# Kernel optimization log

Measured on AMD Instinct MI355X. Metric: run time of the kernel, lower is better.

The kernel has to match this reference:

```python
import jax, jax.numpy as jnp
import numpy as np

B, N, E, D = 4, 4096, 4096, 128
NEG_SLOPE = 0.01
BN_EPS = 1e-5


def setup_inputs() -> dict:
    key = jax.random.key(0)
    ks = jax.random.split(key, 8)
    return {
        "incident_mat": (jax.random.uniform(ks[0], (B, N, E)) < 0.01).astype(jnp.float32),
        "degree_v": jax.random.normal(ks[1], (B, N, N), jnp.float32) * 0.01,
        "degree_e": jax.random.normal(ks[2], (B, E, E), jnp.float32) * 0.01,
        "x": jax.random.normal(ks[3], (B, N, D), jnp.float32),
        "e_masks": jax.random.randint(ks[4], (B, E), 0, 2, jnp.int32),
        "mlp_W": jax.random.normal(ks[5], (D, D), jnp.float32) / np.sqrt(D),
        "mlp_b": jnp.zeros((D,), jnp.float32),
        "theta_att": jax.random.normal(ks[6], (D, 1), jnp.float32) / np.sqrt(D),
        "eps": jax.random.uniform(ks[7], (1,), jnp.float32),
        "bn_gamma": jnp.ones((D,), jnp.float32),
        "bn_beta": jnp.zeros((D,), jnp.float32),
        "bn_mean": jnp.zeros((D,), jnp.float32),
        "bn_var": jnp.ones((D,), jnp.float32),
    }


def reference(incident_mat, degree_v, degree_e, x, e_masks, mlp_W, mlp_b,
              theta_att, eps, bn_gamma, bn_beta, bn_mean, bn_var):
    # MLP (num_mlp_layers=1 -> single Linear)
    x_w = x @ mlp_W + mlp_b                      # [B,N,D]
    Ht = jnp.swapaxes(incident_mat, 1, 2)        # [B,E,N]
    ht_x_w = Ht @ x_w                            # [B,E,D]
    # attention logits per hyperedge
    ht_x_theta = (Ht @ (x @ theta_att))[..., 0]  # [B,E]
    scores = jnp.where(e_masks == 0, -jnp.inf, ht_x_theta)
    attn = jax.nn.softmax(scores, axis=1)        # [B,E]
    # diag_embed + bmm == elementwise row scaling
    h1 = attn[..., None] * ht_x_w                # [B,E,D]
    h1 = incident_mat @ h1                       # [B,N,D]
    h1 = degree_v @ h1                           # [B,N,D]
    h1 = Ht @ h1                                 # [B,E,D]
    h1 = degree_e @ h1                           # [B,E,D]
    h = h1 + eps * ht_x_w                        # [B,E,D]
    h = incident_mat @ h                         # [B,N,D]
    h = jnp.where(h >= 0, h, NEG_SLOPE * h)      # leaky_relu; dropout=identity (eval)
    # BatchNorm1d over channels (inference mode)
    h = (h - bn_mean) / jnp.sqrt(bn_var + BN_EPS) * bn_gamma + bn_beta
    return h
```

## Files before the change

### kernel.cpp

```cpp
#include <hip/hip_runtime.h>


typedef __bf16 bf16;
typedef bf16 bf16x8 __attribute__((ext_vector_type(8)));
typedef float f32x4 __attribute__((ext_vector_type(4)));
typedef unsigned long long u64;
typedef unsigned short u16;
typedef u16 u16x8 __attribute__((ext_vector_type(8)));

#define LDK 72
#define SWZ(r, c) ((c) ^ ((((r) >> 3) & 7) << 3))
#define CAP 192

union BPack { bf16 h[2]; unsigned int u; };
static __device__ __forceinline__ bf16 tob(float f) { return (bf16)f; }

__global__ __launch_bounds__(256) void mlp_k(const float* __restrict__ x,
                                             const float* __restrict__ W,
                                             const float* __restrict__ bias,
                                             const float* __restrict__ theta,
                                             float* __restrict__ xw,
                                             float* __restrict__ xt) {
    __shared__ float Ws[32][128];
    __shared__ float xs[32][128];
    const int t = threadIdx.x;
    const long r0 = (long)blockIdx.x * 32;

    for (int i = t * 4; i < 4096; i += 1024)
        *(float4*)&xs[i >> 7][i & 127] = *(const float4*)&x[r0 * 128 + i];

    const int d = t & 127;
    const int rg = (t >> 7) * 16;
    float acc[16];
#pragma unroll
    for (int r = 0; r < 16; ++r) acc[r] = 0.f;

    for (int kk = 0; kk < 128; kk += 32) {
        __syncthreads();
        for (int i = t * 4; i < 4096; i += 1024)
            *(float4*)&Ws[i >> 7][i & 127] =
                *(const float4*)&W[(kk + (i >> 7)) * 128 + (i & 127)];
        __syncthreads();
        for (int k = 0; k < 32; ++k) {
            float w = Ws[k][d];
#pragma unroll
            for (int r = 0; r < 16; ++r) acc[r] += xs[rg + r][kk + k] * w;
        }
    }
    const float bd = bias[d];
#pragma unroll
    for (int r = 0; r < 16; ++r)
        xw[(r0 + rg + r) * 128 + d] = acc[r] + bd;

    if (t < 32) {
        float s = 0.f;
        for (int k = 0; k < 128; ++k) s += xs[t][k] * theta[k];
        xt[r0 + t] = s;
    }
}

__global__ __launch_bounds__(256) void bmask_lists_k(const float* __restrict__ inc,
                                                     u64* __restrict__ rowmask,
                                                     u16* __restrict__ idx,
                                                     int* __restrict__ cnts) {
    const int b = blockIdx.y;
    const int n = blockIdx.x * 4 + (threadIdx.x >> 6);
    const int l = threadIdx.x & 63;
    const float* p = inc + ((long)b << 24) + (long)n * 4096 + l * 64;
    u64 w = 0;
#pragma unroll
    for (int j = 0; j < 16; ++j) {
        const float4 v = *(const float4*)(p + j * 4);
        w |= (u64)(v.x != 0.f ? 1u : 0u) << (4 * j);
        w |= (u64)(v.y != 0.f ? 1u : 0u) << (4 * j + 1);
        w |= (u64)(v.z != 0.f ? 1u : 0u) << (4 * j + 2);
        w |= (u64)(v.w != 0.f ? 1u : 0u) << (4 * j + 3);
    }
    const long rowid = (long)b * 4096 + n;
    rowmask[rowid * 64 + l] = w;

    const int pc = __popcll(w);
    int pre = pc;
#pragma unroll
    for (int o = 1; o < 64; o <<= 1) {
        int t = __shfl_up(pre, o);
        if (l >= o) pre += t;
    }
    if (l == 63) cnts[rowid] = pre;
    u16* op = idx + rowid * CAP;
    int k = pre - pc;
    u64 m = w;
    while (m) {
        const int bit = __builtin_ctzll(m);
        m &= m - 1;
        if (k < CAP) op[k] = (u16)(l * 64 + bit);
        ++k;
    }
}

__global__ void btrans_k(const u64* __restrict__ rowmask, u64* __restrict__ colmask) {
    const int tn = blockIdx.x, te = blockIdx.y, b = blockIdx.z;
    const int l = threadIdx.x;
    __shared__ u64 w[64];
    w[l] = rowmask[((long)b * 4096 + tn * 64 + l) * 64 + te];
    __syncthreads();
    u64 o = 0;
#pragma unroll 8
    for (int j = 0; j < 64; ++j) o |= ((w[j] >> l) & 1ull) << j;
    colmask[((long)b * 4096 + te * 64 + l) * 64 + tn] = o;
}

__global__ __launch_bounds__(256) void lists_k(const u64* __restrict__ mask,
                                               u16* __restrict__ idx,
                                               int* __restrict__ cnts) {
    const int b = blockIdx.y;
    const int r = blockIdx.x * 4 + (threadIdx.x >> 6);
    const int l = threadIdx.x & 63;
    u64 m = mask[((long)b * 4096 + r) * 64 + l];
    const int pc = __popcll(m);
    int pre = pc;
#pragma unroll
    for (int o = 1; o < 64; o <<= 1) {
        int t = __shfl_up(pre, o);
        if (l >= o) pre += t;
    }
    if (l == 63) cnts[b * 4096 + r] = pre;
    u16* op = idx + ((long)b * 4096 + r) * CAP;
    int k = pre - pc;
    while (m) {
        const int bit = __builtin_ctzll(m);
        m &= m - 1;
        if (k < CAP) op[k] = (u16)(l * 64 + bit);
        ++k;
    }
}

__global__ void softmax_k(const float* __restrict__ sc, const int* __restrict__ mask,
                          float* __restrict__ attn) {
    const int b = blockIdx.x, t = threadIdx.x;
    __shared__ float red[1024];
    const float* sb = sc + b * 4096;
    const int* mb = mask + b * 4096;

    float mx = -1e30f;
    for (int e = t; e < 4096; e += 1024)
        if (mb[e] != 0) mx = fmaxf(mx, sb[e]);
    red[t] = mx;
    __syncthreads();
    for (int st = 512; st > 0; st >>= 1) {
        if (t < st) red[t] = fmaxf(red[t], red[t + st]);
        __syncthreads();
    }
    mx = red[0];
    __syncthreads();

    float sum = 0.f;
    for (int e = t; e < 4096; e += 1024)
        if (mb[e] != 0) sum += expf(sb[e] - mx);
    red[t] = sum;
    __syncthreads();
    for (int st = 512; st > 0; st >>= 1) {
        if (t < st) red[t] += red[t + st];
        __syncthreads();
    }
    const float inv = 1.f / red[0];
    for (int e = t; e < 4096; e += 1024)
        attn[b * 4096 + e] = (mb[e] != 0) ? expf(sb[e] - mx) * inv : 0.f;
}

__global__ __launch_bounds__(256) void scale_k(const float* __restrict__ hxw,
                                               const float* __restrict__ att,
                                               float* __restrict__ outp) {
    const long i4 = (long)blockIdx.x * 256 + threadIdx.x;
    float4 v = ((const float4*)hxw)[i4];
    const float s = att[i4 >> 5];
    v.x *= s; v.y *= s; v.z *= s; v.w *= s;
    ((float4*)outp)[i4] = v;
}

template <int KSP, bool EPS>
__global__ __launch_bounds__(256) void pairsum_k(const float* __restrict__ P,
                                                 const float* __restrict__ H,
                                                 const float* __restrict__ epsp,
                                                 float* __restrict__ O) {
    const long i4 = (long)blockIdx.x * 256 + threadIdx.x;
    float4 a = ((const float4*)P)[i4];
#pragma unroll
    for (int s = 1; s < KSP; ++s) {
        float4 c = ((const float4*)P)[i4 + (long)s * 524288];
        a.x += c.x; a.y += c.y; a.z += c.z; a.w += c.w;
    }
    if (EPS) {
        const float e = epsp[0];
        float4 h = ((const float4*)H)[i4];
        a.x += e * h.x; a.y += e * h.y; a.z += e * h.z; a.w += e * h.w;
    }
    ((float4*)O)[i4] = a;
}

template <bool HXT, bool EPI>
__global__ __launch_bounds__(256) void gatherE_k(
    const u16* __restrict__ idx, const int* __restrict__ cnts,
    const u64* __restrict__ mask, const float* __restrict__ src,
    const float* __restrict__ xt,
    const float* __restrict__ bng, const float* __restrict__ bnb,
    const float* __restrict__ bnm, const float* __restrict__ bnv,
    float* __restrict__ out, float* __restrict__ hxt) {
    const int bid = blockIdx.x;
    const int slot = bid & 7;
    const int b = slot >> 1;
    const int chunk = (bid >> 3) * 2 + (slot & 1);
    const int r = chunk * 4 + (threadIdx.x >> 6);
    const int l = threadIdx.x & 63;
    const long rowid = (long)b * 4096 + r;
    const int cnt = cnts[rowid];
    const u16* ip = idx + rowid * CAP;
    const float* S = src + (long)b * 524288;
    const float* xb = xt + (long)b * 4096;
    const int c0 = 2 * l;

    float ax0 = 0.f, ax1 = 0.f, ax2 = 0.f, ax3 = 0.f;
    float ax4 = 0.f, ax5 = 0.f, ax6 = 0.f, ax7 = 0.f;
    float ay0 = 0.f, ay1 = 0.f, ay2 = 0.f, ay3 = 0.f;
    float ay4 = 0.f, ay5 = 0.f, ay6 = 0.f, ay7 = 0.f;
    float hacc = 0.f;

    const int n = cnt < CAP ? cnt : CAP;
    int i = 0;
    if (n >= 8) {
        u16x8 ia = *(const u16x8*)ip;
        for (; i + 8 <= n; i += 8) {
            const int e0 = ia[0], e1 = ia[1], e2 = ia[2], e3 = ia[3];
            const int e4 = ia[4], e5 = ia[5], e6 = ia[6], e7 = ia[7];
            const float2 v0 = *(const float2*)(S + (long)e0 * 128 + c0);
            const float2 v1 = *(const float2*)(S + (long)e1 * 128 + c0);
            const float2 v2 = *(const float2*)(S + (long)e2 * 128 + c0);
            const float2 v3 = *(const float2*)(S + (long)e3 * 128 + c0);
            const float2 v4 = *(const float2*)(S + (long)e4 * 128 + c0);
            const float2 v5 = *(const float2*)(S + (long)e5 * 128 + c0);
            const float2 v6 = *(const float2*)(S + (long)e6 * 128 + c0);
            const float2 v7 = *(const float2*)(S + (long)e7 * 128 + c0);
            const bool more = (i + 16 <= n);
            u16x8 ib;
            if (more) ib = *(const u16x8*)(ip + i + 8);
            if (HXT)
                hacc += ((xb[e0] + xb[e1]) + (xb[e2] + xb[e3])) +
                        ((xb[e4] + xb[e5]) + (xb[e6] + xb[e7]));
            ax0 += v0.x; ay0 += v0.y; ax1 += v1.x; ay1 += v1.y;
            ax2 += v2.x; ay2 += v2.y; ax3 += v3.x; ay3 += v3.y;
            ax4 += v4.x; ay4 += v4.y; ax5 += v5.x; ay5 += v5.y;
            ax6 += v6.x; ay6 += v6.y; ax7 += v7.x; ay7 += v7.y;
            if (more) ia = ib;
        }
    }
    for (; i < n; ++i) {
        const int e = ip[i];
        const float2 v = *(const float2*)(S + (long)e * 128 + c0);
        if (HXT) hacc += xb[e];
        ax0 += v.x; ay0 += v.y;
    }

    if (cnt > CAP) {
        const u64 wrd = mask[rowid * 64 + l];
        int seen = 0;
        for (int wi = 0; wi < 64; ++wi) {
            u64 m = __shfl(wrd, wi);
            const int pc = __popcll(m);
            if (seen + pc > CAP) {
                int tk = CAP - seen;
                if (tk < 0) tk = 0;
                for (int t = 0; t < tk; ++t) m &= m - 1;
                while (m) {
                    const int bit = __builtin_ctzll(m);
                    m &= m - 1;
                    const int e = (wi << 6) + bit;
                    const float2 v = *(const float2*)(S + (long)e * 128 + c0);
                    if (HXT) hacc += xb[e];
                    ax0 += v.x; ay0 += v.y;
                }
            }
            seen += pc;
        }
    }

    float ax = ((ax0 + ax1) + (ax2 + ax3)) + ((ax4 + ax5) + (ax6 + ax7));
    float ay = ((ay0 + ay1) + (ay2 + ay3)) + ((ay4 + ay5) + (ay6 + ay7));
    if (EPI) {
        float t0 = (ax >= 0.f) ? ax : 0.01f * ax;
        float t1 = (ay >= 0.f) ? ay : 0.01f * ay;
        ax = (t0 - bnm[c0]) * rsqrtf(bnv[c0] + 1e-5f) * bng[c0] + bnb[c0];
        ay = (t1 - bnm[c0 + 1]) * rsqrtf(bnv[c0 + 1] + 1e-5f) * bng[c0 + 1] + bnb[c0 + 1];
    }
    *(float2*)&out[(long)b * 524288 + (long)r * 128 + c0] = (float2){ax, ay};
    if (HXT && l == 0) hxt[rowid] = hacc;
}

template <int KS>
__global__ __launch_bounds__(1024, 4) void gemm_dense(
    const float* __restrict__ A, const float* __restrict__ Bsrc,
    float* __restrict__ P) {
    __shared__ __align__(16) bf16 As[2][128][LDK];
    __shared__ __align__(16) bf16 Bs[2][128][LDK];

    const int tid = threadIdx.x;
    const int bid = blockIdx.x;
    const int slot = bid & 7;
    const int b = slot >> 1;
    const int sub = (bid >> 3) * 2 + (slot & 1);
    const int ksi = sub % KS;
    const int m0 = (sub / KS) * 128;
    constexpr int KCH = 4096 / KS;
    const int kbeg = ksi * KCH, kend = kbeg + KCH;
    const long Aoff = (long)b << 24;
    const long Boff = (long)b * 524288;

    const int wave = tid >> 6, lane = tid & 63;
    const int lr = lane & 15, kb = lane >> 4;
    const int wm = (wave >> 2) * 32, wn = (wave & 3) * 32;

    const int ar = tid >> 3, ak = (tid & 7) * 8;
    const int bd4 = (tid & 31) * 4, bk2 = (tid >> 5) * 2;

    const float* Abase = A + Aoff + (long)(m0 + ar) * 4096 + ak;
    const float* Bbase = Bsrc + Boff + (long)bk2 * 128 + bd4;

    f32x4 acc[2][2];
#pragma unroll
    for (int mf = 0; mf < 2; ++mf)
#pragma unroll
        for (int nf = 0; nf < 2; ++nf) acc[mf][nf] = (f32x4){0.f, 0.f, 0.f, 0.f};

    float4 pa0A, pa1A, pb0A, pb1A;
    float4 pa0B, pa1B, pb0B, pb1B;

#define GLOAD(S, kk)                                                        \
    {                                                                       \
        const float* ga = Abase + (kk);                                     \
        pa0##S = *(const float4*)ga;                                        \
        pa1##S = *(const float4*)(ga + 4);                                  \
        const float* gb = Bbase + (long)(kk) * 128;                         \
        pb0##S = *(const float4*)gb;                                        \
        pb1##S = *(const float4*)(gb + 128);                                \
    }

#define STAGE(S, bu)                                                        \
    {                                                                       \
        bf16x8 p;                                                           \
        p[0] = tob(pa0##S.x); p[1] = tob(pa0##S.y); p[2] = tob(pa0##S.z); p[3] = tob(pa0##S.w); \
        p[4] = tob(pa1##S.x); p[5] = tob(pa1##S.y); p[6] = tob(pa1##S.z); p[7] = tob(pa1##S.w); \
        *(bf16x8*)&As[bu][ar][SWZ(ar, ak)] = p;                             \
        float va[4] = {pb0##S.x, pb0##S.y, pb0##S.z, pb0##S.w};             \
        float vb[4] = {pb1##S.x, pb1##S.y, pb1##S.z, pb1##S.w};             \
        _Pragma("unroll")                                                   \
        for (int j = 0; j < 4; ++j) {                                       \
            BPack q; q.h[0] = tob(va[j]); q.h[1] = tob(vb[j]);              \
            *(unsigned int*)&Bs[bu][bd4 + j][SWZ(bd4 + j, bk2)] = q.u;      \
        }                                                                   \
    }

#define MFMA_STEP(bu)                                                       \
    {                                                                       \
        _Pragma("unroll")                                                   \
        for (int ks = 0; ks < 2; ++ks) {                                    \
            const int ka = ks * 32 + kb * 8;                                \
            bf16x8 af[2], bfr[2];                                           \
            _Pragma("unroll")                                               \
            for (int mf = 0; mf < 2; ++mf) {                                \
                const int rA = wm + mf * 16 + lr;                           \
                af[mf] = *(const bf16x8*)&As[bu][rA][SWZ(rA, ka)];          \
            }                                                               \
            _Pragma("unroll")                                               \
            for (int nf = 0; nf < 2; ++nf) {                                \
                const int rB = wn + nf * 16 + lr;                           \
                bfr[nf] = *(const bf16x8*)&Bs[bu][rB][SWZ(rB, ka)];         \
            }                                                               \
            _Pragma("unroll")                                               \
            for (int mf = 0; mf < 2; ++mf)                                  \
                _Pragma("unroll")                                           \
                for (int nf = 0; nf < 2; ++nf)                              \
                    acc[mf][nf] = __builtin_amdgcn_mfma_f32_16x16x32_bf16(  \
                        af[mf], bfr[nf], acc[mf][nf], 0, 0, 0);             \
        }                                                                   \
    }

    GLOAD(A, kbeg);
    GLOAD(B, kbeg + 64);
    STAGE(A, 0);
    __syncthreads();

    for (int kk = kbeg; kk < kend; kk += 128) {
        MFMA_STEP(0);
        STAGE(B, 1);
        if (kk + 128 < kend) GLOAD(A, kk + 128);
        __syncthreads();
        MFMA_STEP(1);
        if (kk + 128 < kend) {
            STAGE(A, 0);
            if (kk + 192 < kend) GLOAD(B, kk + 192);
            __syncthreads();
        }
    }
#undef GLOAD
#undef STAGE
#undef MFMA_STEP

    float* Cp = P + (long)(ksi * 4 + b) * 524288;
#pragma unroll
    for (int mf = 0; mf < 2; ++mf) {
        const int rb = m0 + wm + mf * 16 + kb * 4;
#pragma unroll
        for (int nf = 0; nf < 2; ++nf) {
            const int col = wn + nf * 16 + lr;
#pragma unroll
            for (int i = 0; i < 4; ++i)
                Cp[(long)(rb + i) * 128 + col] = acc[mf][nf][i];
        }
    }
}

template <int KS>
static void run_all(const float* incident, const float* degree_v, const float* degree_e,
                    const float* x, const int* e_masks, const float* mlp_W,
                    const float* mlp_b, const float* theta, const float* epsp,
                    const float* bng, const float* bnb, const float* bnm,
                    const float* bnv, float* out, float* ws, hipStream_t stream) {
    float* xw    = ws;
    float* hxw   = ws + 2097152;
    float* hxw_s = ws + 4194304;
    float* t1    = ws + 6291456;
    float* Pd    = ws + 8388608;
    float* Psum  = Pd + (long)KS * 2097152;
    float* tail  = Psum + 2097152;
    u64* rowmask = (u64*)tail;
    u64* colmask = rowmask + 1048576;
    u16* rowidx = (u16*)(colmask + 1048576);
    u16* colidx = rowidx + 16384 * CAP;
    int* rowcnt = (int*)(colidx + 16384 * CAP);
    int* colcnt = rowcnt + 16384;
    float* xt  = (float*)(colcnt + 16384);
    float* hxt = xt + 16384;
    float* att = hxt + 16384;

    mlp_k<<<512, 256, 0, stream>>>(x, mlp_W, mlp_b, theta, xw, xt);
    bmask_lists_k<<<dim3(1024, 4), 256, 0, stream>>>(incident, rowmask, rowidx, rowcnt);
    btrans_k<<<dim3(64, 64, 4), 64, 0, stream>>>(rowmask, colmask);
    lists_k<<<dim3(1024, 4), 256, 0, stream>>>(colmask, colidx, colcnt);

    gatherE_k<true, false><<<4096, 256, 0, stream>>>(
        colidx, colcnt, colmask, xw, xt, nullptr, nullptr, nullptr, nullptr,
        hxw, hxt);
    softmax_k<<<4, 1024, 0, stream>>>(hxt, e_masks, att);
    scale_k<<<2048, 256, 0, stream>>>(hxw, att, hxw_s);
    gatherE_k<false, false><<<4096, 256, 0, stream>>>(
        rowidx, rowcnt, rowmask, hxw_s, xt, nullptr, nullptr, nullptr, nullptr,
        t1, nullptr);
    gemm_dense<KS><<<32 * KS * 4, 1024, 0, stream>>>(degree_v, t1, Pd);
    pairsum_k<KS, false><<<2048, 256, 0, stream>>>(Pd, nullptr, nullptr, Psum);
    gatherE_k<false, false><<<4096, 256, 0, stream>>>(
        colidx, colcnt, colmask, Psum, xt, nullptr, nullptr, nullptr, nullptr,
        t1, nullptr);
    gemm_dense<KS><<<32 * KS * 4, 1024, 0, stream>>>(degree_e, t1, Pd);
    pairsum_k<KS, true><<<2048, 256, 0, stream>>>(Pd, hxw, epsp, Psum);
    gatherE_k<false, true><<<4096, 256, 0, stream>>>(
        rowidx, rowcnt, rowmask, Psum, xt, bng, bnb, bnm, bnv, out, nullptr);
}

extern "C" void kernel_launch(void* const* d_in, const int* in_sizes, int n_in,
                              void* d_out, int out_size, void* d_ws, size_t ws_size,
                              hipStream_t stream) {
    const float* incident = (const float*)d_in[0];
    const float* degree_v = (const float*)d_in[1];
    const float* degree_e = (const float*)d_in[2];
    const float* x        = (const float*)d_in[3];
    const int*   e_masks  = (const int*)d_in[4];
    const float* mlp_W    = (const float*)d_in[5];
    const float* mlp_b    = (const float*)d_in[6];
    const float* theta    = (const float*)d_in[7];
    const float* epsp     = (const float*)d_in[8];
    const float* bng      = (const float*)d_in[9];
    const float* bnb      = (const float*)d_in[10];
    const float* bnm      = (const float*)d_in[11];
    const float* bnv      = (const float*)d_in[12];
    float* out = (float*)d_out;
    float* ws = (float*)d_ws;

    if (ws_size >= 130000000ull)
        run_all<4>(incident, degree_v, degree_e, x, e_masks, mlp_W, mlp_b, theta,
                   epsp, bng, bnb, bnm, bnv, out, ws, stream);
    else if (ws_size >= 110000000ull)
        run_all<2>(incident, degree_v, degree_e, x, e_masks, mlp_W, mlp_b, theta,
                   epsp, bng, bnb, bnm, bnv, out, ws, stream);
    else
        run_all<1>(incident, degree_v, degree_e, x, e_masks, mlp_W, mlp_b, theta,
                   epsp, bng, bnb, bnm, bnv, out, ws, stream);
}
```

Before: 416.0 us.

## Use bf16 MFMA for MLP, fuse mask transpose with list build, drop KS=4

```diff
diff --git a/kernel.cpp b/kernel.cpp
--- a/kernel.cpp
+++ b/kernel.cpp
@@ -9,6 +9,7 @@
 typedef u16 u16x8 __attribute__((ext_vector_type(8)));
 
 #define LDK 72
+#define LDM 136
 #define SWZ(r, c) ((c) ^ ((((r) >> 3) & 7) << 3))
 #define CAP 192
 
@@ -21,41 +22,75 @@
                                              const float* __restrict__ theta,
                                              float* __restrict__ xw,
                                              float* __restrict__ xt) {
-    __shared__ float Ws[32][128];
-    __shared__ float xs[32][128];
+    __shared__ __align__(16) bf16 Xs[64][LDM];
+    __shared__ __align__(16) bf16 Ws[128][LDM];
     const int t = threadIdx.x;
-    const long r0 = (long)blockIdx.x * 32;
-
-    for (int i = t * 4; i < 4096; i += 1024)
-        *(float4*)&xs[i >> 7][i & 127] = *(const float4*)&x[r0 * 128 + i];
-
-    const int d = t & 127;
-    const int rg = (t >> 7) * 16;
-    float acc[16];
-#pragma unroll
-    for (int r = 0; r < 16; ++r) acc[r] = 0.f;
-
-    for (int kk = 0; kk < 128; kk += 32) {
-        __syncthreads();
-        for (int i = t * 4; i < 4096; i += 1024)
-            *(float4*)&Ws[i >> 7][i & 127] =
-                *(const float4*)&W[(kk + (i >> 7)) * 128 + (i & 127)];
-        __syncthreads();
-        for (int k = 0; k < 32; ++k) {
-            float w = Ws[k][d];
-#pragma unroll
-            for (int r = 0; r < 16; ++r) acc[r] += xs[rg + r][kk + k] * w;
-        }
-    }
-    const float bd = bias[d];
-#pragma unroll
-    for (int r = 0; r < 16; ++r)
-        xw[(r0 + rg + r) * 128 + d] = acc[r] + bd;
-
-    if (t < 32) {
-        float s = 0.f;
-        for (int k = 0; k < 128; ++k) s += xs[t][k] * theta[k];
-        xt[r0 + t] = s;
+    const long r0 = (long)blockIdx.x * 64;
+
+    {
+        const int row = t >> 2, c = (t & 3) * 32;
+        const float* g = x + (r0 + row) * 128 + c;
+#pragma unroll
+        for (int j8 = 0; j8 < 4; ++j8) {
+            float4 v0 = *(const float4*)(g + j8 * 8);
+            float4 v1 = *(const float4*)(g + j8 * 8 + 4);
+            bf16x8 p;
+            p[0] = tob(v0.x); p[1] = tob(v0.y); p[2] = tob(v0.z); p[3] = tob(v0.w);
+            p[4] = tob(v1.x); p[5] = tob(v1.y); p[6] = tob(v1.z); p[7] = tob(v1.w);
+            *(bf16x8*)&Xs[row][c + j8 * 8] = p;
+        }
+    }
+    {
+        const int wk = t >> 1, wh = (t & 1) * 64;
+        const float* g = W + wk * 128 + wh;
+#pragma unroll
+        for (int j = 0; j < 64; j += 4) {
+            float4 v = *(const float4*)(g + j);
+            Ws[wh + j + 0][wk] = tob(v.x);
+            Ws[wh + j + 1][wk] = tob(v.y);
+            Ws[wh + j + 2][wk] = tob(v.z);
+            Ws[wh + j + 3][wk] = tob(v.w);
+        }
+    }
+    __syncthreads();
+
+    const int wave = t >> 6, lane = t & 63;
+    const int lr = lane & 15, kb = lane >> 4;
+    const int wm = wave * 16;
+
+    f32x4 acc[8];
+#pragma unroll
+    for (int ct = 0; ct < 8; ++ct) acc[ct] = (f32x4){0.f, 0.f, 0.f, 0.f};
+
+#pragma unroll
+    for (int step = 0; step < 4; ++step) {
+        const int ka = step * 32 + kb * 8;
+        bf16x8 af = *(const bf16x8*)&Xs[wm + lr][ka];
+#pragma unroll
+        for (int ct = 0; ct < 8; ++ct) {
+            bf16x8 bfr = *(const bf16x8*)&Ws[ct * 16 + lr][ka];
+            acc[ct] = __builtin_amdgcn_mfma_f32_16x16x32_bf16(af, bfr, acc[ct], 0, 0, 0);
+        }
+    }
+
+    {
+        const int row = t >> 2, q = t & 3;
+        float p = 0.f;
+#pragma unroll
+        for (int kk = 0; kk < 32; ++kk)
+            p += (float)Xs[row][q * 32 + kk] * theta[q * 32 + kk];
+        p += __shfl_down(p, 2);
+        p += __shfl_down(p, 1);
+        if (q == 0) xt[r0 + row] = p;
+    }
+
+#pragma unroll
+    for (int ct = 0; ct < 8; ++ct) {
+        const int col = ct * 16 + lr;
+        const float bd = bias[col];
+#pragma unroll
+        for (int i = 0; i < 4; ++i)
+            xw[(r0 + wm + kb * 4 + i) * 128 + col] = acc[ct][i] + bd;
     }
 }
 
@@ -98,41 +133,35 @@
     }
 }
 
-__global__ void btrans_k(const u64* __restrict__ rowmask, u64* __restrict__ colmask) {
-    const int tn = blockIdx.x, te = blockIdx.y, b = blockIdx.z;
+__global__ __launch_bounds__(64) void btrans_lists_k(const u64* __restrict__ rowmask,
+                                                     u64* __restrict__ colmask,
+                                                     u16* __restrict__ idx,
+                                                     int* __restrict__ cnts) {
+    const int te = blockIdx.x, b = blockIdx.y;
     const int l = threadIdx.x;
     __shared__ u64 w[64];
-    w[l] = rowmask[((long)b * 4096 + tn * 64 + l) * 64 + te];
-    __syncthreads();
-    u64 o = 0;
+    const long rowid = (long)b * 4096 + te * 64 + l;
+    u16* op = idx + rowid * CAP;
+    int k = 0;
+
+    u64 nx = rowmask[((long)b * 4096 + l) * 64 + te];
+    for (int tn = 0; tn < 64; ++tn) {
+        w[l] = nx;
+        __syncthreads();
+        if (tn < 63) nx = rowmask[((long)b * 4096 + (tn + 1) * 64 + l) * 64 + te];
+        u64 o = 0;
 #pragma unroll 8
-    for (int j = 0; j < 64; ++j) o |= ((w[j] >> l) & 1ull) << j;
-    colmask[((long)b * 4096 + te * 64 + l) * 64 + tn] = o;
-}
-
-__global__ __launch_bounds__(256) void lists_k(const u64* __restrict__ mask,
-                                               u16* __restrict__ idx,
-                                               int* __restrict__ cnts) {
-    const int b = blockIdx.y;
-    const int r = blockIdx.x * 4 + (threadIdx.x >> 6);
-    const int l = threadIdx.x & 63;
-    u64 m = mask[((long)b * 4096 + r) * 64 + l];
-    const int pc = __popcll(m);
-    int pre = pc;
-#pragma unroll
-    for (int o = 1; o < 64; o <<= 1) {
-        int t = __shfl_up(pre, o);
-        if (l >= o) pre += t;
-    }
-    if (l == 63) cnts[b * 4096 + r] = pre;
-    u16* op = idx + ((long)b * 4096 + r) * CAP;
-    int k = pre - pc;
-    while (m) {
-        const int bit = __builtin_ctzll(m);
-        m &= m - 1;
-        if (k < CAP) op[k] = (u16)(l * 64 + bit);
-        ++k;
-    }
+        for (int j = 0; j < 64; ++j) o |= ((w[j] >> l) & 1ull) << j;
+        colmask[rowid * 64 + tn] = o;
+        while (o) {
+            const int bit = __builtin_ctzll(o);
+            o &= o - 1;
+            if (k < CAP) op[k] = (u16)(tn * 64 + bit);
+            ++k;
+        }
+        __syncthreads();
+    }
+    cnts[rowid] = k;
 }
 
 __global__ void softmax_k(const float* __restrict__ sc, const int* __restrict__ mask,
@@ -441,10 +470,9 @@
     float* hxt = xt + 16384;
     float* att = hxt + 16384;
 
-    mlp_k<<<512, 256, 0, stream>>>(x, mlp_W, mlp_b, theta, xw, xt);
+    mlp_k<<<256, 256, 0, stream>>>(x, mlp_W, mlp_b, theta, xw, xt);
     bmask_lists_k<<<dim3(1024, 4), 256, 0, stream>>>(incident, rowmask, rowidx, rowcnt);
-    btrans_k<<<dim3(64, 64, 4), 64, 0, stream>>>(rowmask, colmask);
-    lists_k<<<dim3(1024, 4), 256, 0, stream>>>(colmask, colidx, colcnt);
+    btrans_lists_k<<<dim3(64, 4), 64, 0, stream>>>(rowmask, colmask, colidx, colcnt);
 
     gatherE_k<true, false><<<4096, 256, 0, stream>>>(
         colidx, colcnt, colmask, xw, xt, nullptr, nullptr, nullptr, nullptr,
@@ -484,10 +512,7 @@
     float* out = (float*)d_out;
     float* ws = (float*)d_ws;
 
-    if (ws_size >= 130000000ull)
-        run_all<4>(incident, degree_v, degree_e, x, e_masks, mlp_W, mlp_b, theta,
-                   epsp, bng, bnb, bnm, bnv, out, ws, stream);
-    else if (ws_size >= 110000000ull)
+    if (ws_size >= 110000000ull)
         run_all<2>(incident, degree_v, degree_e, x, e_masks, mlp_W, mlp_b, theta,
                    epsp, bng, bnb, bnm, bnv, out, ws, stream);
     else
```

Result: slower. 443.4 us (+6.6%).
